# Kernel tuning notes

Hardware: AMD Instinct MI355X
Metric: run time of the kernel (lower is better)

## Reference

```python
import jax, jax.numpy as jnp
import numpy as np

HEADS = 16
EPS = 1e-6


def setup_inputs() -> dict:
    key = jax.random.key(0)
    k1, k2, k3 = jax.random.split(key, 3)
    B, N, C = 4, 4096, 1024
    x = jax.random.normal(k1, (B, N, C), dtype=jnp.float32)
    w_qkv = jax.random.normal(k2, (3 * C, C), dtype=jnp.float32) * (C ** -0.5)
    w_out = jax.random.normal(k3, (C, C), dtype=jnp.float32) * (C ** -0.5)
    b_out = jnp.zeros((C,), dtype=jnp.float32)
    return {"x": x, "w_qkv": w_qkv, "w_out": w_out, "b_out": b_out}


def reference(x, w_qkv, w_out, b_out):
    B, N, C = x.shape
    H = HEADS
    D = C // H
    scale = D ** -0.25

    qkv = x @ w_qkv.T  # [B, N, 3C]
    q, k, v = jnp.split(qkv, 3, axis=-1)

    def heads(t):  # [B, N, C] -> [B, H, N, D]
        return t.reshape(B, N, H, D).transpose(0, 2, 1, 3)

    q, k, v = heads(q), heads(k), heads(v)

    feat = lambda t: jax.nn.elu(t) + 1.0
    q = feat(q) * scale
    k = feat(k) * scale

    kv = jnp.einsum('bhnd,bhne->bhde', k, v)      # [B, H, D, D]
    out = jnp.einsum('bhnd,bhde->bhne', q, kv)    # [B, H, N, D]
    k_sum = k.sum(axis=2)                          # [B, H, D]
    denom = jnp.einsum('bhnd,bhd->bhn', q, k_sum)  # [B, H, N]
    out = out / (denom[..., None] + EPS)

    out = out.transpose(0, 2, 1, 3).reshape(B, N, C)
    return out @ w_out.T + b_out
```

## Files before the change

kernel.cpp:

```cpp
#include <hip/hip_runtime.h>
#include <hip/hip_bf16.h>
#include <cmath>


typedef __bf16 bf16_t;
typedef __attribute__((ext_vector_type(8))) __bf16 bf16x8;
typedef __attribute__((ext_vector_type(4))) __bf16 bf16x4;
typedef __attribute__((ext_vector_type(4))) float f32x4;
typedef __attribute__((ext_vector_type(8))) float f32x8;
typedef __attribute__((ext_vector_type(16))) float f32x16;

#define MFMA16(a, b, c) __builtin_amdgcn_mfma_f32_16x16x32_bf16((a), (b), (c), 0, 0, 0)
#define MFMA32(a, b, c) __builtin_amdgcn_mfma_f32_32x32x16_bf16((a), (b), (c), 0, 0, 0)

#define LDS_PITCH 72

__device__ __forceinline__ f32x4 zf4() { f32x4 z; z[0] = 0.f; z[1] = 0.f; z[2] = 0.f; z[3] = 0.f; return z; }

__device__ __forceinline__ float feat(float x) { return x > 0.f ? x + 1.f : expf(x); }

__device__ __forceinline__ void gld_lds16(const bf16_t* src, bf16_t* dst)
{
    __builtin_amdgcn_global_load_lds(
        (__attribute__((address_space(1))) void*)const_cast<bf16_t*>(src),
        (__attribute__((address_space(3))) void*)dst, 16, 0, 0);
}

template <int NR>
__device__ __forceinline__ void stage_async(const bf16_t* g, int ld, bf16_t* lds, int tid)
{
    const int w = tid >> 6, l = tid & 63;
    constexpr int CALLS = NR >> 5;
#pragma unroll
    for (int p = 0; p < CALLS; ++p) {
        const int chunk = w * CALLS + p;
        const int gidx = chunk * 64 + l;
        const int row = gidx >> 3;
        const int cp = gidx & 7;
        const int c = cp ^ (row & 7);
        gld_lds16(g + row * ld + c * 8, lds + chunk * 512);
    }
}

__device__ __forceinline__ bf16x8 read_frag_sw(const bf16_t* lds, int row, int cg)
{
    const int sw = cg ^ (row & 7);
    return *(const bf16x8*)(lds + row * 64 + sw * 8);
}

__global__ __launch_bounds__(256) void cvt_all_kernel(
    const float* __restrict__ x, bf16_t* __restrict__ xb,
    const float* __restrict__ wqkv, bf16_t* __restrict__ wqkvb,
    const float* __restrict__ wout, bf16_t* __restrict__ woutb)
{
    const int g = blockIdx.x * 256 + threadIdx.x;
    const float* src;
    bf16_t* dst;
    size_t off;
    if (g < 2097152)      { src = x;    dst = xb;    off = (size_t)g * 8; }
    else if (g < 2490368) { src = wqkv; dst = wqkvb; off = (size_t)(g - 2097152) * 8; }
    else                  { src = wout; dst = woutb; off = (size_t)(g - 2490368) * 8; }
    f32x8 f = *(const f32x8*)(src + off);
    bf16x8 v;
#pragma unroll
    for (int t = 0; t < 8; ++t) v[t] = (bf16_t)f[t];
    *(bf16x8*)(dst + off) = v;
}

template <int MODE>
__global__ __launch_bounds__(256, 3) void gemm_bt_kernel(
    const bf16_t* __restrict__ A, const bf16_t* __restrict__ B, int K,
    void* __restrict__ out0, bf16_t* __restrict__ out1, bf16_t* __restrict__ out2,
    const float* __restrict__ bias)
{
    __shared__ __align__(16) bf16_t As[128 * 64];
    __shared__ __align__(16) bf16_t Bs[128 * 64];
    const int tid = threadIdx.x;
    const int l = tid & 63, w = tid >> 6;
    const int wm = w >> 1, wn = w & 1;
    const int lid = l & 31, half = l >> 5;
    const int m0 = blockIdx.y * 128;
    const int n0 = blockIdx.x * 128;

    f32x16 acc[2][2];
#pragma unroll
    for (int i = 0; i < 2; ++i)
#pragma unroll
        for (int j = 0; j < 2; ++j)
#pragma unroll
            for (int r = 0; r < 16; ++r) acc[i][j][r] = 0.f;

    const bf16_t* Ab = A + (size_t)m0 * K;
    const bf16_t* Bb = B + (size_t)n0 * K;

    for (int k0 = 0; k0 < K; k0 += 64) {
        stage_async<128>(Ab + k0, K, As, tid);
        stage_async<128>(Bb + k0, K, Bs, tid);
        __syncthreads();
#pragma unroll
        for (int s = 0; s < 4; ++s) {
            const int cg = s * 2 + half;
            bf16x8 af[2], bfr[2];
#pragma unroll
            for (int i = 0; i < 2; ++i) af[i] = read_frag_sw(As, wm * 64 + i * 32 + lid, cg);
#pragma unroll
            for (int j = 0; j < 2; ++j) bfr[j] = read_frag_sw(Bs, wn * 64 + j * 32 + lid, cg);
#pragma unroll
            for (int i = 0; i < 2; ++i)
#pragma unroll
                for (int j = 0; j < 2; ++j)
                    acc[i][j] = MFMA32(af[i], bfr[j], acc[i][j]);
        }
        __syncthreads();
    }

    const float scale = 0.3535533905932738f;
#pragma unroll
    for (int i = 0; i < 2; ++i) {
        const int rowb = m0 + wm * 64 + i * 32 + 4 * half;
#pragma unroll
        for (int j = 0; j < 2; ++j) {
            const int col = n0 + wn * 64 + j * 32 + lid;
            if (MODE == 1) {
                float* yp = (float*)out0;
                const float bb = bias[col];
#pragma unroll
                for (int r = 0; r < 16; ++r) {
                    const int row = rowb + (r & 3) + 8 * (r >> 2);
                    yp[(size_t)row * 1024 + col] = acc[i][j][r] + bb;
                }
            } else {
                const int part = col >> 10;
                const int cc = col & 1023;
                const int hh = (rowb >> 12) * 16 + (cc >> 6);
                const int d = cc & 63;
                if (part == 0) {
                    bf16_t* qp = (bf16_t*)out0 + ((size_t)hh * 4096) * 64 + d;
#pragma unroll
                    for (int r = 0; r < 16; ++r) {
                        const int ntok = (rowb + (r & 3) + 8 * (r >> 2)) & 4095;
                        qp[(size_t)ntok * 64] = (bf16_t)(feat(acc[i][j][r]) * scale);
                    }
                } else {
                    bf16_t* tp = (part == 1 ? out1 : out2) + ((size_t)hh * 64 + d) * 4096;
#pragma unroll
                    for (int rg = 0; rg < 4; ++rg) {
                        const int ntok = (rowb + 8 * rg) & 4095;
                        bf16x4 pk;
#pragma unroll
                        for (int r = 0; r < 4; ++r) {
                            float v = acc[i][j][rg * 4 + r];
                            if (part == 1) v = feat(v) * scale;
                            pk[r] = (bf16_t)v;
                        }
                        *(bf16x4*)(tp + ntok) = pk;
                    }
                }
            }
        }
    }
}

__global__ __launch_bounds__(256) void kv_partial_kernel(
    const bf16_t* __restrict__ KT, const bf16_t* __restrict__ VT,
    float* __restrict__ kvp, float* __restrict__ ksp_out)
{
    const int tid = threadIdx.x;
    const int l = tid & 63, w = tid >> 6;
    const int quad = l >> 4, r16 = l & 15;
    const int hh = blockIdx.x;
    const int ksp = blockIdx.y;
    const bf16_t* kb = KT + (size_t)hh * 64 * 4096 + ksp * 1024;
    const bf16_t* vb = VT + (size_t)hh * 64 * 4096 + ksp * 1024;

    bf16x8 ones;
#pragma unroll
    for (int t = 0; t < 8; ++t) ones[t] = (bf16_t)1.0f;

    f32x4 acc[4], accks[4];
#pragma unroll
    for (int j = 0; j < 4; ++j) { acc[j] = zf4(); accks[j] = zf4(); }

#pragma unroll 4
    for (int kc = 0; kc < 32; ++kc) {
        const int koff = kc * 32 + quad * 8;
        const bf16x8 af = *(const bf16x8*)(vb + (size_t)(w * 16 + r16) * 4096 + koff);
        bf16x8 bk[4];
#pragma unroll
        for (int j = 0; j < 4; ++j)
            bk[j] = *(const bf16x8*)(kb + (size_t)(j * 16 + r16) * 4096 + koff);
#pragma unroll
        for (int j = 0; j < 4; ++j) acc[j] = MFMA16(af, bk[j], acc[j]);
        if (w == 0) {
#pragma unroll
            for (int j = 0; j < 4; ++j) accks[j] = MFMA16(ones, bk[j], accks[j]);
        }
    }

    float* ob = kvp + (size_t)(hh * 4 + ksp) * 4096;
    const int ebase = w * 16 + quad * 4;
#pragma unroll
    for (int j = 0; j < 4; ++j)
#pragma unroll
        for (int r = 0; r < 4; ++r)
            ob[(ebase + r) * 64 + j * 16 + r16] = acc[j][r];

    if (w == 0 && quad == 0) {
        float* kso = ksp_out + (size_t)(hh * 4 + ksp) * 64;
#pragma unroll
        for (int j = 0; j < 4; ++j) kso[j * 16 + r16] = accks[j][0];
    }
}

__global__ __launch_bounds__(256) void kvfix_kernel(
    const float* __restrict__ kvp, const float* __restrict__ ksp,
    bf16_t* __restrict__ kvb, bf16_t* __restrict__ ksumb)
{
    const int hh = blockIdx.x, t = threadIdx.x;
    const float* base = kvp + (size_t)hh * 4 * 4096;
    const int off = t * 16;
    bf16x8 o[2];
#pragma unroll
    for (int c = 0; c < 4; ++c) {
        f32x4 s = *(const f32x4*)(base + off + c * 4);
        s += *(const f32x4*)(base + 4096 + off + c * 4);
        s += *(const f32x4*)(base + 8192 + off + c * 4);
        s += *(const f32x4*)(base + 12288 + off + c * 4);
#pragma unroll
        for (int r = 0; r < 4; ++r) o[c >> 1][(c & 1) * 4 + r] = (bf16_t)s[r];
    }
    *(bf16x8*)(kvb + (size_t)hh * 4096 + off) = o[0];
    *(bf16x8*)(kvb + (size_t)hh * 4096 + off + 8) = o[1];
    if (t < 64) {
        const float* kb = ksp + (size_t)hh * 4 * 64;
        ksumb[(size_t)hh * 64 + t] = (bf16_t)(kb[t] + kb[64 + t] + kb[128 + t] + kb[192 + t]);
    }
}

__global__ __launch_bounds__(256, 2) void attn_out_kernel(
    const bf16_t* __restrict__ Q, const bf16_t* __restrict__ kvb, const bf16_t* __restrict__ ksumb,
    bf16_t* __restrict__ att)
{
    __shared__ __align__(16) bf16_t kvT[64 * LDS_PITCH];
    __shared__ __align__(16) bf16_t ksb[64];
    const int tid = threadIdx.x;
    const int l = tid & 63, w = tid >> 6;
    const int quad = l >> 4, r16 = l & 15;
    const int hh = blockIdx.x;
    const int b = hh >> 4, h = hh & 15;
    const int mt = blockIdx.y;

    {
        const int e = tid >> 2, d0 = (tid & 3) * 16;
        const bf16_t* kvbh = kvb + (size_t)hh * 4096;
        *(bf16x8*)(kvT + e * LDS_PITCH + d0)     = *(const bf16x8*)(kvbh + e * 64 + d0);
        *(bf16x8*)(kvT + e * LDS_PITCH + d0 + 8) = *(const bf16x8*)(kvbh + e * 64 + d0 + 8);
        if (tid < 64) ksb[tid] = ksumb[(size_t)hh * 64 + tid];
    }
    __syncthreads();

    f32x4 acc[4][4];
    f32x4 dacc[4];
#pragma unroll
    for (int i = 0; i < 4; ++i) {
        dacc[i] = zf4();
#pragma unroll
        for (int j = 0; j < 4; ++j) acc[i][j] = zf4();
    }

    const int m0w = mt * 256 + w * 64;
    const bf16_t* qb = Q + (size_t)hh * 4096 * 64;
#pragma unroll
    for (int ks = 0; ks < 2; ++ks) {
        bf16x8 kf = *(const bf16x8*)(ksb + ks * 32 + quad * 8);
        if (r16 != 0) {
#pragma unroll
            for (int t = 0; t < 8; ++t) kf[t] = (bf16_t)0.f;
        }
        bf16x8 bfr[4];
#pragma unroll
        for (int j = 0; j < 4; ++j)
            bfr[j] = *(const bf16x8*)(kvT + (j * 16 + r16) * LDS_PITCH + ks * 32 + quad * 8);
#pragma unroll
        for (int i = 0; i < 4; ++i) {
            const bf16_t* qp = qb + (size_t)(m0w + i * 16 + r16) * 64 + ks * 32 + quad * 8;
            const bf16x8 af = *(const bf16x8*)qp;
            dacc[i] = MFMA16(af, kf, dacc[i]);
#pragma unroll
            for (int j = 0; j < 4; ++j) acc[i][j] = MFMA16(af, bfr[j], acc[i][j]);
        }
    }

#pragma unroll
    for (int i = 0; i < 4; ++i) {
        float den[4];
#pragma unroll
        for (int r = 0; r < 4; ++r)
            den[r] = __shfl(dacc[i][r], l & 48) + 1e-6f;
#pragma unroll
        for (int j = 0; j < 4; ++j) {
            const size_t colb = (size_t)h * 64 + j * 16 + r16;
#pragma unroll
            for (int r = 0; r < 4; ++r) {
                const int ntok = m0w + i * 16 + quad * 4 + r;
                att[((size_t)b * 4096 + ntok) * 1024 + colb] = (bf16_t)(acc[i][j][r] / den[r]);
            }
        }
    }
}

extern "C" void kernel_launch(void* const* d_in, const int* in_sizes, int n_in,
                              void* d_out, int out_size, void* d_ws, size_t ws_size,
                              hipStream_t stream)
{
    const float* x    = (const float*)d_in[0];
    const float* wqkv = (const float*)d_in[1];
    const float* wout = (const float*)d_in[2];
    const float* bout = (const float*)d_in[3];
    float* y = (float*)d_out;

    char* ws = (char*)d_ws;
    bf16_t* xb    = (bf16_t*)ws;
    bf16_t* wqkvb = (bf16_t*)(ws + (size_t)32 * 1048576);
    bf16_t* woutb = (bf16_t*)(ws + (size_t)38 * 1048576);
    bf16_t* Q     = (bf16_t*)(ws + (size_t)40 * 1048576);
    bf16_t* KT    = (bf16_t*)(ws + (size_t)72 * 1048576);
    bf16_t* VT    = (bf16_t*)(ws + (size_t)104 * 1048576);
    float* kvp    = (float*)ws;
    float* ksp    = (float*)(ws + (size_t)4 * 1048576);
    bf16_t* kvb   = (bf16_t*)(ws + (size_t)5 * 1048576);
    bf16_t* ksumb = (bf16_t*)(ws + (size_t)6 * 1048576);
    bf16_t* att   = KT;

    cvt_all_kernel<<<10240, 256, 0, stream>>>(x, xb, wqkv, wqkvb, wout, woutb);

    gemm_bt_kernel<0><<<dim3(24, 128), 256, 0, stream>>>(xb, wqkvb, 1024, Q, KT, VT, nullptr);
    kv_partial_kernel<<<dim3(64, 4), 256, 0, stream>>>(KT, VT, kvp, ksp);
    kvfix_kernel<<<64, 256, 0, stream>>>(kvp, ksp, kvb, ksumb);
    attn_out_kernel<<<dim3(64, 16), 256, 0, stream>>>(Q, kvb, ksumb, att);
    gemm_bt_kernel<1><<<dim3(8, 128), 256, 0, stream>>>(att, woutb, 1024, y, nullptr, nullptr, bout);
}
```

Before: 345.5 us.

## Switch GEMM to 16x16 MFMA and split QKV GEMM with swapped operands for K/V

Replaces the 32x32x16 MFMA tiling with 16x16x32 MFMA (4x4 accumulators per wave) in the shared GEMM kernel. The QKV projection is split into two launches: Q keeps the normal layout, while K/V use swapped MFMA operands so each lane holds consecutive tokens for the transposed KT/VT stores. The aim is a different MFMA throughput and fragment-read pattern, and simpler epilogue indexing. In exchange the K/V epilogue now writes single bf16 scalars with a per-element part/head computation instead of packed 4-wide stores, and there is one extra kernel launch.

```diff
diff --git a/kernel.cpp b/kernel.cpp
--- a/kernel.cpp
+++ b/kernel.cpp
@@ -8,10 +8,8 @@
 typedef __attribute__((ext_vector_type(4))) __bf16 bf16x4;
 typedef __attribute__((ext_vector_type(4))) float f32x4;
 typedef __attribute__((ext_vector_type(8))) float f32x8;
-typedef __attribute__((ext_vector_type(16))) float f32x16;
 
 #define MFMA16(a, b, c) __builtin_amdgcn_mfma_f32_16x16x32_bf16((a), (b), (c), 0, 0, 0)
-#define MFMA32(a, b, c) __builtin_amdgcn_mfma_f32_32x32x16_bf16((a), (b), (c), 0, 0, 0)
 
 #define LDS_PITCH 72
 
@@ -67,9 +65,9 @@
     *(bf16x8*)(dst + off) = v;
 }
 
-template <int MODE>
+template <int MODE, int SWAP>
 __global__ __launch_bounds__(256, 3) void gemm_bt_kernel(
-    const bf16_t* __restrict__ A, const bf16_t* __restrict__ B, int K,
+    const bf16_t* __restrict__ A, const bf16_t* __restrict__ B, int K, int n_off,
     void* __restrict__ out0, bf16_t* __restrict__ out1, bf16_t* __restrict__ out2,
     const float* __restrict__ bias)
 {
@@ -78,17 +76,15 @@
     const int tid = threadIdx.x;
     const int l = tid & 63, w = tid >> 6;
     const int wm = w >> 1, wn = w & 1;
-    const int lid = l & 31, half = l >> 5;
+    const int quad = l >> 4, r16 = l & 15;
     const int m0 = blockIdx.y * 128;
-    const int n0 = blockIdx.x * 128;
-
-    f32x16 acc[2][2];
-#pragma unroll
-    for (int i = 0; i < 2; ++i)
-#pragma unroll
-        for (int j = 0; j < 2; ++j)
-#pragma unroll
-            for (int r = 0; r < 16; ++r) acc[i][j][r] = 0.f;
+    const int n0 = (blockIdx.x + n_off) * 128;
+
+    f32x4 acc[4][4];
+#pragma unroll
+    for (int i = 0; i < 4; ++i)
+#pragma unroll
+        for (int j = 0; j < 4; ++j) acc[i][j] = zf4();
 
     const bf16_t* Ab = A + (size_t)m0 * K;
     const bf16_t* Bb = B + (size_t)n0 * K;
@@ -98,64 +94,72 @@
         stage_async<128>(Bb + k0, K, Bs, tid);
         __syncthreads();
 #pragma unroll
-        for (int s = 0; s < 4; ++s) {
-            const int cg = s * 2 + half;
-            bf16x8 af[2], bfr[2];
-#pragma unroll
-            for (int i = 0; i < 2; ++i) af[i] = read_frag_sw(As, wm * 64 + i * 32 + lid, cg);
-#pragma unroll
-            for (int j = 0; j < 2; ++j) bfr[j] = read_frag_sw(Bs, wn * 64 + j * 32 + lid, cg);
-#pragma unroll
-            for (int i = 0; i < 2; ++i)
-#pragma unroll
-                for (int j = 0; j < 2; ++j)
-                    acc[i][j] = MFMA32(af[i], bfr[j], acc[i][j]);
+        for (int ks = 0; ks < 2; ++ks) {
+            const int cg = ks * 4 + quad;
+            bf16x8 af[4], bfr[4];
+#pragma unroll
+            for (int i = 0; i < 4; ++i) af[i] = read_frag_sw(As, wm * 64 + i * 16 + r16, cg);
+#pragma unroll
+            for (int j = 0; j < 4; ++j) bfr[j] = read_frag_sw(Bs, wn * 64 + j * 16 + r16, cg);
+#pragma unroll
+            for (int i = 0; i < 4; ++i)
+#pragma unroll
+                for (int j = 0; j < 4; ++j) {
+                    if (SWAP == 0)
+                        acc[i][j] = MFMA16(af[i], bfr[j], acc[i][j]);
+                    else
+                        acc[i][j] = MFMA16(bfr[j], af[i], acc[i][j]);
+                }
         }
         __syncthreads();
     }
 
     const float scale = 0.3535533905932738f;
-#pragma unroll
-    for (int i = 0; i < 2; ++i) {
-        const int rowb = m0 + wm * 64 + i * 32 + 4 * half;
-#pragma unroll
-        for (int j = 0; j < 2; ++j) {
-            const int col = n0 + wn * 64 + j * 32 + lid;
+    if (SWAP == 1) {
+#pragma unroll
+        for (int i = 0; i < 4; ++i) {
+            const int tb = m0 + wm * 64 + i * 16;
+            const int bq = tb >> 12;
+            const int t4 = (tb & 4095) + r16;
+#pragma unroll
+            for (int j = 0; j < 4; ++j) {
+                const int colb = n0 + wn * 64 + j * 16 + quad * 4;
+#pragma unroll
+                for (int r = 0; r < 4; ++r) {
+                    const int c = colb + r;
+                    const int part = c >> 10;
+                    const int cc = c & 1023;
+                    const int hh = bq * 16 + (cc >> 6);
+                    const int d = cc & 63;
+                    float v = acc[i][j][r];
+                    if (part == 1) v = feat(v) * scale;
+                    bf16_t* tp = (part == 1 ? out1 : out2) + ((size_t)hh * 64 + d) * 4096 + t4;
+                    *tp = (bf16_t)v;
+                }
+            }
+        }
+        return;
+    }
+#pragma unroll
+    for (int i = 0; i < 4; ++i) {
+        const int mbase = m0 + wm * 64 + i * 16 + quad * 4;
+#pragma unroll
+        for (int j = 0; j < 4; ++j) {
+            const int col = n0 + wn * 64 + j * 16 + r16;
             if (MODE == 1) {
                 float* yp = (float*)out0;
                 const float bb = bias[col];
 #pragma unroll
-                for (int r = 0; r < 16; ++r) {
-                    const int row = rowb + (r & 3) + 8 * (r >> 2);
-                    yp[(size_t)row * 1024 + col] = acc[i][j][r] + bb;
-                }
+                for (int r = 0; r < 4; ++r)
+                    yp[(size_t)(mbase + r) * 1024 + col] = acc[i][j][r] + bb;
             } else {
-                const int part = col >> 10;
-                const int cc = col & 1023;
-                const int hh = (rowb >> 12) * 16 + (cc >> 6);
-                const int d = cc & 63;
-                if (part == 0) {
-                    bf16_t* qp = (bf16_t*)out0 + ((size_t)hh * 4096) * 64 + d;
-#pragma unroll
-                    for (int r = 0; r < 16; ++r) {
-                        const int ntok = (rowb + (r & 3) + 8 * (r >> 2)) & 4095;
-                        qp[(size_t)ntok * 64] = (bf16_t)(feat(acc[i][j][r]) * scale);
-                    }
-                } else {
-                    bf16_t* tp = (part == 1 ? out1 : out2) + ((size_t)hh * 64 + d) * 4096;
-#pragma unroll
-                    for (int rg = 0; rg < 4; ++rg) {
-                        const int ntok = (rowb + 8 * rg) & 4095;
-                        bf16x4 pk;
-#pragma unroll
-                        for (int r = 0; r < 4; ++r) {
-                            float v = acc[i][j][rg * 4 + r];
-                            if (part == 1) v = feat(v) * scale;
-                            pk[r] = (bf16_t)v;
-                        }
-                        *(bf16x4*)(tp + ntok) = pk;
-                    }
-                }
+                const int hh = (mbase >> 12) * 16 + (col >> 6);
+                const int d = col & 63;
+                const int ntok = mbase & 4095;
+                bf16_t* qp = (bf16_t*)out0 + ((size_t)hh * 4096 + ntok) * 64 + d;
+#pragma unroll
+                for (int r = 0; r < 4; ++r)
+                    qp[(size_t)r * 64] = (bf16_t)(feat(acc[i][j][r]) * scale);
             }
         }
     }
@@ -334,9 +338,10 @@
 
     cvt_all_kernel<<<10240, 256, 0, stream>>>(x, xb, wqkv, wqkvb, wout, woutb);
 
-    gemm_bt_kernel<0><<<dim3(24, 128), 256, 0, stream>>>(xb, wqkvb, 1024, Q, KT, VT, nullptr);
+    gemm_bt_kernel<0, 0><<<dim3(8, 128), 256, 0, stream>>>(xb, wqkvb, 1024, 0, Q, nullptr, nullptr, nullptr);
+    gemm_bt_kernel<0, 1><<<dim3(16, 128), 256, 0, stream>>>(xb, wqkvb, 1024, 8, nullptr, KT, VT, nullptr);
     kv_partial_kernel<<<dim3(64, 4), 256, 0, stream>>>(KT, VT, kvp, ksp);
     kvfix_kernel<<<64, 256, 0, stream>>>(kvp, ksp, kvb, ksumb);
     attn_out_kernel<<<dim3(64, 16), 256, 0, stream>>>(Q, kvb, ksumb, att);
-    gemm_bt_kernel<1><<<dim3(8, 128), 256, 0, stream>>>(att, woutb, 1024, y, nullptr, nullptr, bout);
-}
+    gemm_bt_kernel<1, 0><<<dim3(8, 128), 256, 0, stream>>>(att, woutb, 1024, 0, y, nullptr, nullptr, bout);
+}
```

Measured after the change: 355.5 us. 1.03x slower.
